# Kernel optimization log

Hardware: AMD Instinct MI355X
Metric: run time of the kernel (lower is better)

The kernel has to match this reference:

```python
import jax, jax.numpy as jnp
import numpy as np

N_NODES = 100000
N_EDGES = 1600000
HIDDEN = 128
N_CLASSES = 40
# torch.rand(1).item() in apply_randalign; fixed here for a deterministic reference
ALPHA = 0.62


def setup_inputs() -> dict:
    key = jax.random.key(0)
    ks = jax.random.split(key, 6)
    inputs = jax.random.normal(ks[0], (N_NODES, HIDDEN), jnp.float32)
    src = jax.random.randint(ks[1], (N_EDGES,), 0, N_NODES, jnp.int32)
    dst = jax.random.randint(ks[2], (N_EDGES,), 0, N_NODES, jnp.int32)
    s = 1.0 / np.sqrt(HIDDEN)
    W1 = jax.random.normal(ks[3], (HIDDEN, HIDDEN), jnp.float32) * s
    W2 = jax.random.normal(ks[4], (HIDDEN, HIDDEN), jnp.float32) * s
    W3 = jax.random.normal(ks[5], (HIDDEN, N_CLASSES), jnp.float32) * s
    return dict(inputs=inputs, src=src, dst=dst,
                W1=W1, b1=jnp.zeros((HIDDEN,), jnp.float32),
                W2=W2, b2=jnp.zeros((HIDDEN,), jnp.float32),
                W3=W3, b3=jnp.zeros((N_CLASSES,), jnp.float32))


def _graph_conv(x, W, b, src, dst):
    # DGL GraphConv, norm='both': D_dst^{-1/2} A D_src^{-1/2} X W + b
    n = x.shape[0]
    ones = jnp.ones(src.shape, x.dtype)
    deg_out = jnp.clip(jax.ops.segment_sum(ones, src, num_segments=n), 1.0)
    deg_in = jnp.clip(jax.ops.segment_sum(ones, dst, num_segments=n), 1.0)
    h = (x @ W) * (deg_out ** -0.5)[:, None]          # row scaling commutes with XW
    agg = jax.ops.segment_sum(h[src], dst, num_segments=n)
    return agg * (deg_in ** -0.5)[:, None] + b


def _randalign(h_prev, h_curr, alpha):
    norm_prev = jnp.linalg.norm(h_prev, axis=1, keepdims=True)
    norm_curr = jnp.linalg.norm(h_curr, axis=1, keepdims=True)
    scaled_prev = h_prev * (norm_curr / norm_prev)
    return alpha * h_curr + (1.0 - alpha) * scaled_prev


def reference(inputs, src, dst, W1, b1, W2, b2, W3, b3):
    # Faithful to source: layers[0] is never applied; loop runs over layers[1..-2].
    h = jax.nn.relu(_graph_conv(inputs, W1, b1, src, dst))      # i = 1
    h_next = jax.nn.relu(_graph_conv(h, W2, b2, src, dst))      # i = 2
    h = _randalign(h, h_next, ALPHA)
    logits = _graph_conv(h, W3, b3, src, dst)                   # final layer
    return logits
```

## Files before the change

kernel.cpp:

```cpp
#include <hip/hip_runtime.h>
#include <hip/hip_bf16.h>

#define HIDDEN 128
#define ALPHA_F 0.62f
#define CAP 64
#define BKT_BITS 9
#define BCAP 10240
#define CSTRIDE 136

typedef __attribute__((ext_vector_type(8))) short bf16x8;
typedef __attribute__((ext_vector_type(4))) float f32x4;

__device__ inline unsigned short f2bf(float f) {
  unsigned u = __float_as_uint(f);
  unsigned r = (u + 0x7fffu + ((u >> 16) & 1u)) >> 16;
  return (unsigned short)r;
}
__device__ inline float bf2f(unsigned short h) {
  return __uint_as_float((unsigned)h << 16);
}
__device__ inline float bflo(unsigned x) { return __uint_as_float(x << 16); }
__device__ inline float bfhi(unsigned x) { return __uint_as_float(x & 0xffff0000u); }
__device__ inline unsigned bfpack(float a, float b) {
  return (unsigned)f2bf(a) | ((unsigned)f2bf(b) << 16);
}

__device__ inline f32x4 mfma_bf16(bf16x8 a, bf16x8 b, f32x4 c) {
  return __builtin_amdgcn_mfma_f32_16x16x32_bf16(a, b, c, 0, 0, 0);
}

template <int CT>
__device__ void gemm_mfma_body(const float* __restrict__ A,
                               const unsigned short* __restrict__ WhT,
                               const unsigned short* __restrict__ WlT,
                               unsigned short* __restrict__ outp, int n, int NW, int gi,
                               unsigned* __restrict__ smem) {
  unsigned short* s16 = (unsigned short*)smem;
  const int t = threadIdx.x;
  const int wv = t >> 6, l = t & 63;
  const int lr = l & 15, lg = (l >> 4) & 3;
  const int rb = gi * 128;

  constexpr int WSLOTS = 4 * CT * 64;
  for (int s = t; s < WSLOTS; s += 256) {
    int sl = s & 63;
    int cc = s >> 6;
    int ct = cc % CT, c = cc / CT;
    int col = ct * 16 + (sl & 15);
    int k = c * 32 + ((sl >> 4) & 3) * 8;
    uint4 hv = *(const uint4*)&WhT[(size_t)col * HIDDEN + k];
    uint4 lv = *(const uint4*)&WlT[(size_t)col * HIDDEN + k];
    *(uint4*)&s16[(cc * 2 + 0) * 512 + sl * 8] = hv;
    *(uint4*)&s16[(cc * 2 + 1) * 512 + sl * 8] = lv;
  }

  f32x4 acc[2][CT];
#pragma unroll
  for (int rt = 0; rt < 2; rt++)
#pragma unroll
    for (int ct = 0; ct < CT; ct++)
#pragma unroll
      for (int e = 0; e < 4; e++) acc[rt][ct][e] = 0.f;

  __syncthreads();

  for (int c = 0; c < 4; c++) {
    bf16x8 ah[2], al[2];
#pragma unroll
    for (int rt = 0; rt < 2; rt++) {
      int rr = rb + wv * 32 + rt * 16 + lr;
      if (rr >= n) rr = n - 1;
      const float4* g = (const float4*)(A + (size_t)rr * HIDDEN + c * 32 + lg * 8);
      float4 v0 = g[0], v1 = g[1];
      float f[8] = {v0.x, v0.y, v0.z, v0.w, v1.x, v1.y, v1.z, v1.w};
#pragma unroll
      for (int q = 0; q < 8; q++) {
        unsigned short h = f2bf(f[q]);
        ah[rt][q] = (short)h;
        al[rt][q] = (short)f2bf(f[q] - bf2f(h));
      }
    }
#pragma unroll
    for (int ct = 0; ct < CT; ct++) {
      int cc = c * CT + ct;
      bf16x8 bh = *(const bf16x8*)&s16[(cc * 2 + 0) * 512 + l * 8];
      bf16x8 bl = *(const bf16x8*)&s16[(cc * 2 + 1) * 512 + l * 8];
#pragma unroll
      for (int rt = 0; rt < 2; rt++) {
        acc[rt][ct] = mfma_bf16(ah[rt], bh, acc[rt][ct]);
        acc[rt][ct] = mfma_bf16(al[rt], bh, acc[rt][ct]);
        acc[rt][ct] = mfma_bf16(ah[rt], bl, acc[rt][ct]);
      }
    }
  }

  __syncthreads();
  unsigned short* cr = s16 + wv * (32 * CSTRIDE);
#pragma unroll
  for (int rt = 0; rt < 2; rt++)
#pragma unroll
    for (int ct = 0; ct < CT; ct++)
#pragma unroll
      for (int r = 0; r < 4; r++)
        cr[(rt * 16 + lg * 4 + r) * CSTRIDE + ct * 16 + lr] = f2bf(acc[rt][ct][r]);
#pragma unroll
  for (int ps = 0; ps < 8; ps++) {
    int row_local = ps * 4 + lg;
    int orow = rb + wv * 32 + row_local;
    if (orow < n && lr * 8 < NW) {
      uint4 v = *(const uint4*)&cr[row_local * CSTRIDE + lr * 8];
      *(uint4*)&outp[(size_t)orow * NW + lr * 8] = v;
    }
  }
}

template <int CT>
__device__ void gemm_bf16A_body(const unsigned short* __restrict__ A,
                                const unsigned short* __restrict__ WhT,
                                const unsigned short* __restrict__ WlT,
                                unsigned short* __restrict__ outp, int n, int NW, int gi,
                                unsigned* __restrict__ smem) {
  unsigned short* s16 = (unsigned short*)smem;
  const int t = threadIdx.x;
  const int wv = t >> 6, l = t & 63;
  const int lr = l & 15, lg = (l >> 4) & 3;
  const int rb = gi * 128;

  constexpr int WSLOTS = 4 * CT * 64;
  for (int s = t; s < WSLOTS; s += 256) {
    int sl = s & 63;
    int cc = s >> 6;
    int ct = cc % CT, c = cc / CT;
    int col = ct * 16 + (sl & 15);
    int k = c * 32 + ((sl >> 4) & 3) * 8;
    uint4 hv = *(const uint4*)&WhT[(size_t)col * HIDDEN + k];
    uint4 lv = *(const uint4*)&WlT[(size_t)col * HIDDEN + k];
    *(uint4*)&s16[(cc * 2 + 0) * 512 + sl * 8] = hv;
    *(uint4*)&s16[(cc * 2 + 1) * 512 + sl * 8] = lv;
  }

  f32x4 acc[2][CT];
#pragma unroll
  for (int rt = 0; rt < 2; rt++)
#pragma unroll
    for (int ct = 0; ct < CT; ct++)
#pragma unroll
      for (int e = 0; e < 4; e++) acc[rt][ct][e] = 0.f;

  __syncthreads();

  for (int c = 0; c < 4; c++) {
    bf16x8 ah[2];
#pragma unroll
    for (int rt = 0; rt < 2; rt++) {
      int rr = rb + wv * 32 + rt * 16 + lr;
      if (rr >= n) rr = n - 1;
      ah[rt] = *(const bf16x8*)&A[(size_t)rr * HIDDEN + c * 32 + lg * 8];
    }
#pragma unroll
    for (int ct = 0; ct < CT; ct++) {
      int cc = c * CT + ct;
      bf16x8 bh = *(const bf16x8*)&s16[(cc * 2 + 0) * 512 + l * 8];
      bf16x8 bl = *(const bf16x8*)&s16[(cc * 2 + 1) * 512 + l * 8];
#pragma unroll
      for (int rt = 0; rt < 2; rt++) {
        acc[rt][ct] = mfma_bf16(ah[rt], bh, acc[rt][ct]);
        acc[rt][ct] = mfma_bf16(ah[rt], bl, acc[rt][ct]);
      }
    }
  }

  __syncthreads();
  unsigned short* cr = s16 + wv * (32 * CSTRIDE);
#pragma unroll
  for (int rt = 0; rt < 2; rt++)
#pragma unroll
    for (int ct = 0; ct < CT; ct++)
#pragma unroll
      for (int r = 0; r < 4; r++)
        cr[(rt * 16 + lg * 4 + r) * CSTRIDE + ct * 16 + lr] = f2bf(acc[rt][ct][r]);
#pragma unroll
  for (int ps = 0; ps < 8; ps++) {
    int row_local = ps * 4 + lg;
    int orow = rb + wv * 32 + row_local;
    if (orow < n && lr * 8 < NW) {
      uint4 v = *(const uint4*)&cr[row_local * CSTRIDE + lr * 8];
      *(uint4*)&outp[(size_t)orow * NW + lr * 8] = v;
    }
  }
}

__global__ __launch_bounds__(256) void partition_kernel(
    const int* __restrict__ src, const int* __restrict__ dst, int E, int nbkt,
    unsigned* __restrict__ gcur1, unsigned* __restrict__ gcur2,
    unsigned* __restrict__ stg1, unsigned short* __restrict__ stg2, int pa_blocks,
    const float* __restrict__ W1, const float* __restrict__ W2, const float* __restrict__ W3,
    unsigned short* __restrict__ W1h, unsigned short* __restrict__ W1l,
    unsigned short* __restrict__ W2h, unsigned short* __restrict__ W2l,
    unsigned short* __restrict__ W3h, unsigned short* __restrict__ W3l, int NC) {
  const int t = threadIdx.x;
  const int bid = blockIdx.x;
  if (bid >= pa_blocks) {
    int r = bid - pa_blocks;
    const float* W = (r == 0) ? W1 : (r == 1) ? W2 : W3;
    unsigned short* Wh = (r == 0) ? W1h : (r == 1) ? W2h : W3h;
    unsigned short* Wl = (r == 0) ? W1l : (r == 1) ? W2l : W3l;
    int ncol = (r == 2) ? 64 : 128;
    int nw   = (r == 2) ? NC : 128;
    for (int idx = t; idx < ncol * HIDDEN; idx += 256) {
      int c = idx >> 7, k = idx & 127;
      float v = (c < nw) ? W[(size_t)k * nw + c] : 0.f;
      unsigned short hi = f2bf(v);
      Wh[idx] = hi;
      Wl[idx] = f2bf(v - bf2f(hi));
    }
    return;
  }
  __shared__ unsigned h1[256], h2[256], b1[256], b2[256];
  h1[t] = 0; h2[t] = 0;
  __syncthreads();
  const int chunk = (E + pa_blocks - 1) / pa_blocks;
  const int e0 = bid * chunk, e1 = min(e0 + chunk, E);
  for (int e = e0 + t; e < e1; e += 256) {
    atomicAdd(&h1[(unsigned)dst[e] >> BKT_BITS], 1u);
    atomicAdd(&h2[(unsigned)src[e] >> BKT_BITS], 1u);
  }
  __syncthreads();
  if (t < nbkt) {
    b1[t] = atomicAdd(&gcur1[t], h1[t]);
    b2[t] = atomicAdd(&gcur2[t], h2[t]);
  }
  h1[t] = 0; h2[t] = 0;
  __syncthreads();
  for (int e = e0 + t; e < e1; e += 256) {
    int s = src[e], d = dst[e];
    unsigned bk1 = (unsigned)d >> BKT_BITS;
    unsigned p1 = b1[bk1] + atomicAdd(&h1[bk1], 1u);
    if (p1 < BCAP) stg1[(size_t)bk1 * BCAP + p1] = ((unsigned)s << BKT_BITS) | ((unsigned)d & 511u);
    unsigned bk2 = (unsigned)s >> BKT_BITS;
    unsigned p2 = b2[bk2] + atomicAdd(&h2[bk2], 1u);
    if (p2 < BCAP) stg2[(size_t)bk2 * BCAP + p2] = (unsigned short)(s & 511);
  }
}

__global__ __launch_bounds__(256) void csr_and_gemm1_kernel(
    const unsigned* __restrict__ gcur1, const unsigned* __restrict__ gcur2,
    const unsigned* __restrict__ stg1, const unsigned short* __restrict__ stg2,
    int* __restrict__ csr, int* __restrict__ deg_in, int* __restrict__ deg_out,
    int n, int nbkt,
    const float* __restrict__ X,
    const unsigned short* __restrict__ W1h, const unsigned short* __restrict__ W1l,
    unsigned short* __restrict__ T1) {
  __shared__ __align__(16) unsigned smem[16384];
  const int bid = blockIdx.x;
  if (bid >= 2 * nbkt) {
    gemm_mfma_body<8>(X, W1h, W1l, T1, n, HIDDEN, bid - 2 * nbkt, smem);
    return;
  }
  int* cnt = (int*)smem;
  const int t = threadIdx.x;
  cnt[t] = 0; cnt[t + 256] = 0;
  __syncthreads();
  if (bid < nbkt) {
    const int b = bid;
    const int m = min((int)gcur1[b], BCAP);
    const int node0 = b << BKT_BITS;
    for (int i = t; i < m; i += 256) {
      unsigned val = stg1[(size_t)b * BCAP + i];
      int dl = val & 511;
      int s = (int)(val >> BKT_BITS);
      int pos = atomicAdd(&cnt[dl], 1);
      if (pos < CAP) csr[((size_t)(node0 + dl) << 6) + pos] = s;
    }
    __syncthreads();
    for (int u = t; u < 512; u += 256) {
      int node = node0 + u;
      if (node < n) deg_in[node] = cnt[u];
    }
  } else {
    const int b = bid - nbkt;
    const int m = min((int)gcur2[b], BCAP);
    const int node0 = b << BKT_BITS;
    for (int i = t; i < m; i += 256) {
      atomicAdd(&cnt[stg2[(size_t)b * BCAP + i]], 1);
    }
    __syncthreads();
    for (int u = t; u < 512; u += 256) {
      int node = node0 + u;
      if (node < n) deg_out[node] = cnt[u];
    }
  }
}

__global__ __launch_bounds__(256) void gemm2_kernel(
    const unsigned short* __restrict__ A,
    const unsigned short* __restrict__ Wh, const unsigned short* __restrict__ Wl,
    unsigned short* __restrict__ T, int n) {
  __shared__ __align__(16) unsigned smem[16384];
  gemm_bf16A_body<8>(A, Wh, Wl, T, n, HIDDEN, blockIdx.x, smem);
}

__global__ __launch_bounds__(256) void gemm3_kernel(
    const unsigned short* __restrict__ A,
    const unsigned short* __restrict__ Wh, const unsigned short* __restrict__ Wl,
    unsigned short* __restrict__ T, int n) {
  __shared__ __align__(16) unsigned smem[9000];
  gemm_bf16A_body<4>(A, Wh, Wl, T, n, 64, blockIdx.x, smem);
}

template <bool RA>
__global__ __launch_bounds__(256) void gather_conv_kernel(
    const uint4* __restrict__ Tr, const int* __restrict__ csr,
    const int* __restrict__ deg_out, const int* __restrict__ deg_in,
    const float* __restrict__ bias, unsigned short* H, int n) {
  const int wv = threadIdx.x >> 6, l = threadIdx.x & 63;
  const int v = blockIdx.x * 4 + wv;
  if (v >= n) return;
  const int q = l >> 4, cg = l & 15;
  const int deg = deg_in[v];
  const int m = min(deg, CAP);
  int iu = (l < m) ? csr[((size_t)v << 6) + l] : 0;
  float wu = (l < m) ? rsqrtf((float)max(deg_out[iu], 1)) : 0.f;

  float a0 = 0.f, a1 = 0.f, a2 = 0.f, a3 = 0.f, a4 = 0.f, a5 = 0.f, a6 = 0.f, a7 = 0.f;
  float b0 = 0.f, b1 = 0.f, b2 = 0.f, b3 = 0.f, b4 = 0.f, b5 = 0.f, b6 = 0.f, b7 = 0.f;
  int j = 0;
  for (; j + 8 <= m; j += 8) {
    int eA = j + q, eB = j + 4 + q;
    int uA = __shfl(iu, eA), uB = __shfl(iu, eB);
    float wA = __shfl(wu, eA), wB = __shfl(wu, eB);
    uint4 xA = Tr[(size_t)uA * 16 + cg];
    uint4 xB = Tr[(size_t)uB * 16 + cg];
    a0 = fmaf(wA, bflo(xA.x), a0); a1 = fmaf(wA, bfhi(xA.x), a1);
    a2 = fmaf(wA, bflo(xA.y), a2); a3 = fmaf(wA, bfhi(xA.y), a3);
    a4 = fmaf(wA, bflo(xA.z), a4); a5 = fmaf(wA, bfhi(xA.z), a5);
    a6 = fmaf(wA, bflo(xA.w), a6); a7 = fmaf(wA, bfhi(xA.w), a7);
    b0 = fmaf(wB, bflo(xB.x), b0); b1 = fmaf(wB, bfhi(xB.x), b1);
    b2 = fmaf(wB, bflo(xB.y), b2); b3 = fmaf(wB, bfhi(xB.y), b3);
    b4 = fmaf(wB, bflo(xB.z), b4); b5 = fmaf(wB, bfhi(xB.z), b5);
    b6 = fmaf(wB, bflo(xB.w), b6); b7 = fmaf(wB, bfhi(xB.w), b7);
  }
  for (; j < m; j += 4) {
    int e = j + q;
    int u = __shfl(iu, e);
    float w = __shfl(wu, e);
    uint4 x = Tr[(size_t)u * 16 + cg];
    a0 = fmaf(w, bflo(x.x), a0); a1 = fmaf(w, bfhi(x.x), a1);
    a2 = fmaf(w, bflo(x.y), a2); a3 = fmaf(w, bfhi(x.y), a3);
    a4 = fmaf(w, bflo(x.z), a4); a5 = fmaf(w, bfhi(x.z), a5);
    a6 = fmaf(w, bflo(x.w), a6); a7 = fmaf(w, bfhi(x.w), a7);
  }
  a0 += b0; a1 += b1; a2 += b2; a3 += b3; a4 += b4; a5 += b5; a6 += b6; a7 += b7;
#pragma unroll
  for (int off = 16; off < 64; off <<= 1) {
    a0 += __shfl_xor(a0, off); a1 += __shfl_xor(a1, off);
    a2 += __shfl_xor(a2, off); a3 += __shfl_xor(a3, off);
    a4 += __shfl_xor(a4, off); a5 += __shfl_xor(a5, off);
    a6 += __shfl_xor(a6, off); a7 += __shfl_xor(a7, off);
  }

  float din = rsqrtf((float)max(deg, 1));
  float4 bA = ((const float4*)bias)[cg * 2];
  float4 bB = ((const float4*)bias)[cg * 2 + 1];
  float r0 = fmaxf(a0 * din + bA.x, 0.f);
  float r1 = fmaxf(a1 * din + bA.y, 0.f);
  float r2 = fmaxf(a2 * din + bA.z, 0.f);
  float r3 = fmaxf(a3 * din + bA.w, 0.f);
  float r4 = fmaxf(a4 * din + bB.x, 0.f);
  float r5 = fmaxf(a5 * din + bB.y, 0.f);
  float r6 = fmaxf(a6 * din + bB.z, 0.f);
  float r7 = fmaxf(a7 * din + bB.w, 0.f);

  if (RA) {
    uint4 hp = ((const uint4*)(H + (size_t)v * HIDDEN))[cg];
    float p0 = bflo(hp.x), p1 = bfhi(hp.x), p2 = bflo(hp.y), p3 = bfhi(hp.y);
    float p4 = bflo(hp.z), p5 = bfhi(hp.z), p6 = bflo(hp.w), p7 = bfhi(hp.w);
    float sc = r0*r0 + r1*r1 + r2*r2 + r3*r3 + r4*r4 + r5*r5 + r6*r6 + r7*r7;
    float sp = p0*p0 + p1*p1 + p2*p2 + p3*p3 + p4*p4 + p5*p5 + p6*p6 + p7*p7;
#pragma unroll
    for (int off = 1; off < 16; off <<= 1) {
      sc += __shfl_xor(sc, off);
      sp += __shfl_xor(sp, off);
    }
    float ratio = sqrtf(sc) / sqrtf(sp);
    const float am = 1.0f - ALPHA_F;
    r0 = ALPHA_F * r0 + am * p0 * ratio; r1 = ALPHA_F * r1 + am * p1 * ratio;
    r2 = ALPHA_F * r2 + am * p2 * ratio; r3 = ALPHA_F * r3 + am * p3 * ratio;
    r4 = ALPHA_F * r4 + am * p4 * ratio; r5 = ALPHA_F * r5 + am * p5 * ratio;
    r6 = ALPHA_F * r6 + am * p6 * ratio; r7 = ALPHA_F * r7 + am * p7 * ratio;
  }
  if (q == 0) {
    uint4 pk = make_uint4(bfpack(r0, r1), bfpack(r2, r3), bfpack(r4, r5), bfpack(r6, r7));
    ((uint4*)(H + (size_t)v * HIDDEN))[cg] = pk;
  }
}

__global__ __launch_bounds__(256) void gather_final_kernel(
    const uint4* __restrict__ Tr3, const int* __restrict__ csr,
    const int* __restrict__ deg_out, const int* __restrict__ deg_in,
    const float* __restrict__ bias, float* __restrict__ out, int n, int NC) {
  const int wv = threadIdx.x >> 6, l = threadIdx.x & 63;
  const int v = blockIdx.x * 4 + wv;
  if (v >= n) return;
  const int o = l >> 3, cg = l & 7;
  const int deg = deg_in[v];
  const int m = min(deg, CAP);
  int iu = (l < m) ? csr[((size_t)v << 6) + l] : 0;
  float wu = (l < m) ? rsqrtf((float)max(deg_out[iu], 1)) : 0.f;

  float a0 = 0.f, a1 = 0.f, a2 = 0.f, a3 = 0.f, a4 = 0.f, a5 = 0.f, a6 = 0.f, a7 = 0.f;
  float b0 = 0.f, b1 = 0.f, b2 = 0.f, b3 = 0.f, b4 = 0.f, b5 = 0.f, b6 = 0.f, b7 = 0.f;
  int j = 0;
  for (; j + 16 <= m; j += 16) {
    int eA = j + o, eB = j + 8 + o;
    int uA = __shfl(iu, eA), uB = __shfl(iu, eB);
    float wA = __shfl(wu, eA), wB = __shfl(wu, eB);
    uint4 xA = Tr3[(size_t)uA * 8 + cg];
    uint4 xB = Tr3[(size_t)uB * 8 + cg];
    a0 = fmaf(wA, bflo(xA.x), a0); a1 = fmaf(wA, bfhi(xA.x), a1);
    a2 = fmaf(wA, bflo(xA.y), a2); a3 = fmaf(wA, bfhi(xA.y), a3);
    a4 = fmaf(wA, bflo(xA.z), a4); a5 = fmaf(wA, bfhi(xA.z), a5);
    a6 = fmaf(wA, bflo(xA.w), a6); a7 = fmaf(wA, bfhi(xA.w), a7);
    b0 = fmaf(wB, bflo(xB.x), b0); b1 = fmaf(wB, bfhi(xB.x), b1);
    b2 = fmaf(wB, bflo(xB.y), b2); b3 = fmaf(wB, bfhi(xB.y), b3);
    b4 = fmaf(wB, bflo(xB.z), b4); b5 = fmaf(wB, bfhi(xB.z), b5);
    b6 = fmaf(wB, bflo(xB.w), b6); b7 = fmaf(wB, bfhi(xB.w), b7);
  }
  for (; j < m; j += 8) {
    int e = j + o;
    int u = __shfl(iu, e);
    float w = __shfl(wu, e);
    uint4 x = Tr3[(size_t)u * 8 + cg];
    a0 = fmaf(w, bflo(x.x), a0); a1 = fmaf(w, bfhi(x.x), a1);
    a2 = fmaf(w, bflo(x.y), a2); a3 = fmaf(w, bfhi(x.y), a3);
    a4 = fmaf(w, bflo(x.z), a4); a5 = fmaf(w, bfhi(x.z), a5);
    a6 = fmaf(w, bflo(x.w), a6); a7 = fmaf(w, bfhi(x.w), a7);
  }
  a0 += b0; a1 += b1; a2 += b2; a3 += b3; a4 += b4; a5 += b5; a6 += b6; a7 += b7;
#pragma unroll
  for (int off = 8; off < 64; off <<= 1) {
    a0 += __shfl_xor(a0, off); a1 += __shfl_xor(a1, off);
    a2 += __shfl_xor(a2, off); a3 += __shfl_xor(a3, off);
    a4 += __shfl_xor(a4, off); a5 += __shfl_xor(a5, off);
    a6 += __shfl_xor(a6, off); a7 += __shfl_xor(a7, off);
  }
  if (l < 5) {
    float din = rsqrtf((float)max(deg, 1));
    float4 bA = ((const float4*)bias)[l * 2];
    float4 bB = ((const float4*)bias)[l * 2 + 1];
    float4 oA = make_float4(a0 * din + bA.x, a1 * din + bA.y, a2 * din + bA.z, a3 * din + bA.w);
    float4 oB = make_float4(a4 * din + bB.x, a5 * din + bB.y, a6 * din + bB.z, a7 * din + bB.w);
    *(float4*)(out + (size_t)v * NC + 8 * l) = oA;
    *(float4*)(out + (size_t)v * NC + 8 * l + 4) = oB;
  }
}

extern "C" void kernel_launch(void* const* d_in, const int* in_sizes, int n_in,
                              void* d_out, int out_size, void* d_ws, size_t ws_size,
                              hipStream_t stream) {
  const float* X  = (const float*)d_in[0];
  const int* src  = (const int*)d_in[1];
  const int* dst  = (const int*)d_in[2];
  const float* W1 = (const float*)d_in[3];
  const float* b1 = (const float*)d_in[4];
  const float* W2 = (const float*)d_in[5];
  const float* b2 = (const float*)d_in[6];
  const float* W3 = (const float*)d_in[7];
  const float* b3 = (const float*)d_in[8];
  float* out = (float*)d_out;

  const int n = in_sizes[0] / HIDDEN;
  const int E = in_sizes[1];
  const int NC = in_sizes[8];
  const int nbkt = (n + 511) >> BKT_BITS;

  char* p = (char*)d_ws;
  auto alloc = [&](size_t bytes) {
    char* r = p;
    p += (bytes + 255) & ~(size_t)255;
    return r;
  };
  unsigned* gcur1 = (unsigned*)alloc(512 * 4);
  unsigned* gcur2 = gcur1 + 256;
  int* deg_out    = (int*)alloc((size_t)n * 4);
  int* deg_in     = (int*)alloc((size_t)n * 4);
  int* csr        = (int*)alloc((size_t)n * CAP * 4);
  unsigned short* stg2 = (unsigned short*)alloc((size_t)256 * BCAP * 2);
  unsigned* stg1  = (unsigned*)alloc((size_t)256 * BCAP * 4);
  unsigned short* BufT = (unsigned short*)alloc((size_t)n * HIDDEN * 2);
  unsigned short* BufH = (unsigned short*)alloc((size_t)n * HIDDEN * 2);
  unsigned short* W1h = (unsigned short*)alloc(128 * 128 * 2);
  unsigned short* W1l = (unsigned short*)alloc(128 * 128 * 2);
  unsigned short* W2h = (unsigned short*)alloc(128 * 128 * 2);
  unsigned short* W2l = (unsigned short*)alloc(128 * 128 * 2);
  unsigned short* W3h = (unsigned short*)alloc(64 * 128 * 2);
  unsigned short* W3l = (unsigned short*)alloc(64 * 128 * 2);

  hipMemsetAsync(gcur1, 0, 512 * 4, stream);

  const int PA = 256;
  partition_kernel<<<PA + 3, 256, 0, stream>>>(src, dst, E, nbkt, gcur1, gcur2, stg1, stg2, PA,
                                               W1, W2, W3, W1h, W1l, W2h, W2l, W3h, W3l, NC);

  int gb = (n + 127) / 128;
  csr_and_gemm1_kernel<<<2 * nbkt + gb, 256, 0, stream>>>(gcur1, gcur2, stg1, stg2,
                                                          csr, deg_in, deg_out, n, nbkt,
                                                          X, W1h, W1l, BufT);
  int hb = (n + 3) / 4;
  gather_conv_kernel<false><<<hb, 256, 0, stream>>>(
      (const uint4*)BufT, csr, deg_out, deg_in, b1, BufH, n);
  gemm2_kernel<<<gb, 256, 0, stream>>>(BufH, W2h, W2l, BufT, n);
  gather_conv_kernel<true><<<hb, 256, 0, stream>>>(
      (const uint4*)BufT, csr, deg_out, deg_in, b2, BufH, n);
  gemm3_kernel<<<gb, 256, 0, stream>>>(BufH, W3h, W3l, BufT, n);
  gather_final_kernel<<<hb, 256, 0, stream>>>(
      (const uint4*)BufT, csr, deg_out, deg_in, b3, out, n, NC);
}
```

Baseline: 277.5 us.

## Fold source-degree scaling into GEMM epilogues and rework gathers to per-edge wave loads

Adds a kernel that precomputes per-node deg_out^-1/2 once. The gemm2 and gemm3 epilogues now apply that scale to rows before storing, so the layer-2 and layer-3 gathers become plain sums. The gather kernels are restructured so the whole wave reads one neighbor row per step, with the index broadcast via readlane, instead of splitting lanes across edges and reducing with shuffles. This removes per-edge rsqrt work and the cross-lane reductions, but each wave now issues narrower 4-byte or 2-byte loads per edge with less memory-level parallelism. It also adds one extra launch.

```diff
diff --git a/kernel.cpp b/kernel.cpp
--- a/kernel.cpp
+++ b/kernel.cpp
@@ -118,6 +118,7 @@
 __device__ void gemm_bf16A_body(const unsigned short* __restrict__ A,
                                 const unsigned short* __restrict__ WhT,
                                 const unsigned short* __restrict__ WlT,
+                                const float* __restrict__ dsc,
                                 unsigned short* __restrict__ outp, int n, int NW, int gi,
                                 unsigned* __restrict__ smem) {
   unsigned short* s16 = (unsigned short*)smem;
@@ -173,12 +174,16 @@
   __syncthreads();
   unsigned short* cr = s16 + wv * (32 * CSTRIDE);
 #pragma unroll
-  for (int rt = 0; rt < 2; rt++)
-#pragma unroll
-    for (int ct = 0; ct < CT; ct++)
-#pragma unroll
-      for (int r = 0; r < 4; r++)
-        cr[(rt * 16 + lg * 4 + r) * CSTRIDE + ct * 16 + lr] = f2bf(acc[rt][ct][r]);
+  for (int rt = 0; rt < 2; rt++) {
+#pragma unroll
+    for (int r = 0; r < 4; r++) {
+      int orow = rb + wv * 32 + rt * 16 + lg * 4 + r;
+      float sc = dsc[min(orow, n - 1)];
+#pragma unroll
+      for (int ct = 0; ct < CT; ct++)
+        cr[(rt * 16 + lg * 4 + r) * CSTRIDE + ct * 16 + lr] = f2bf(acc[rt][ct][r] * sc);
+    }
+  }
 #pragma unroll
   for (int ps = 0; ps < 8; ps++) {
     int row_local = ps * 4 + lg;
@@ -292,166 +297,126 @@
   }
 }
 
+__global__ __launch_bounds__(256) void dscale_kernel(const int* __restrict__ deg_out,
+                                                     float* __restrict__ dscale, int n) {
+  int i = blockIdx.x * 256 + threadIdx.x;
+  if (i < n) dscale[i] = rsqrtf((float)max(deg_out[i], 1));
+}
+
 __global__ __launch_bounds__(256) void gemm2_kernel(
     const unsigned short* __restrict__ A,
     const unsigned short* __restrict__ Wh, const unsigned short* __restrict__ Wl,
-    unsigned short* __restrict__ T, int n) {
+    const float* __restrict__ dsc, unsigned short* __restrict__ T, int n) {
   __shared__ __align__(16) unsigned smem[16384];
-  gemm_bf16A_body<8>(A, Wh, Wl, T, n, HIDDEN, blockIdx.x, smem);
+  gemm_bf16A_body<8>(A, Wh, Wl, dsc, T, n, HIDDEN, blockIdx.x, smem);
 }
 
 __global__ __launch_bounds__(256) void gemm3_kernel(
     const unsigned short* __restrict__ A,
     const unsigned short* __restrict__ Wh, const unsigned short* __restrict__ Wl,
-    unsigned short* __restrict__ T, int n) {
+    const float* __restrict__ dsc, unsigned short* __restrict__ T, int n) {
   __shared__ __align__(16) unsigned smem[9000];
-  gemm_bf16A_body<4>(A, Wh, Wl, T, n, 64, blockIdx.x, smem);
-}
-
-template <bool RA>
+  gemm_bf16A_body<4>(A, Wh, Wl, dsc, T, n, 64, blockIdx.x, smem);
+}
+
+template <bool APPLYW, bool RA>
 __global__ __launch_bounds__(256) void gather_conv_kernel(
-    const uint4* __restrict__ Tr, const int* __restrict__ csr,
-    const int* __restrict__ deg_out, const int* __restrict__ deg_in,
+    const unsigned* __restrict__ Tu, const int* __restrict__ csr,
+    const float* __restrict__ dscale, const int* __restrict__ deg_in,
     const float* __restrict__ bias, unsigned short* H, int n) {
-  const int wv = threadIdx.x >> 6, l = threadIdx.x & 63;
-  const int v = blockIdx.x * 4 + wv;
+  const int l = threadIdx.x & 63;
+  const int v = __builtin_amdgcn_readfirstlane(blockIdx.x * 4 + (threadIdx.x >> 6));
   if (v >= n) return;
-  const int q = l >> 4, cg = l & 15;
   const int deg = deg_in[v];
   const int m = min(deg, CAP);
   int iu = (l < m) ? csr[((size_t)v << 6) + l] : 0;
-  float wu = (l < m) ? rsqrtf((float)max(deg_out[iu], 1)) : 0.f;
-
-  float a0 = 0.f, a1 = 0.f, a2 = 0.f, a3 = 0.f, a4 = 0.f, a5 = 0.f, a6 = 0.f, a7 = 0.f;
-  float b0 = 0.f, b1 = 0.f, b2 = 0.f, b3 = 0.f, b4 = 0.f, b5 = 0.f, b6 = 0.f, b7 = 0.f;
-  int j = 0;
-  for (; j + 8 <= m; j += 8) {
-    int eA = j + q, eB = j + 4 + q;
-    int uA = __shfl(iu, eA), uB = __shfl(iu, eB);
-    float wA = __shfl(wu, eA), wB = __shfl(wu, eB);
-    uint4 xA = Tr[(size_t)uA * 16 + cg];
-    uint4 xB = Tr[(size_t)uB * 16 + cg];
-    a0 = fmaf(wA, bflo(xA.x), a0); a1 = fmaf(wA, bfhi(xA.x), a1);
-    a2 = fmaf(wA, bflo(xA.y), a2); a3 = fmaf(wA, bfhi(xA.y), a3);
-    a4 = fmaf(wA, bflo(xA.z), a4); a5 = fmaf(wA, bfhi(xA.z), a5);
-    a6 = fmaf(wA, bflo(xA.w), a6); a7 = fmaf(wA, bfhi(xA.w), a7);
-    b0 = fmaf(wB, bflo(xB.x), b0); b1 = fmaf(wB, bfhi(xB.x), b1);
-    b2 = fmaf(wB, bflo(xB.y), b2); b3 = fmaf(wB, bfhi(xB.y), b3);
-    b4 = fmaf(wB, bflo(xB.z), b4); b5 = fmaf(wB, bfhi(xB.z), b5);
-    b6 = fmaf(wB, bflo(xB.w), b6); b7 = fmaf(wB, bfhi(xB.w), b7);
-  }
-  for (; j < m; j += 4) {
-    int e = j + q;
-    int u = __shfl(iu, e);
-    float w = __shfl(wu, e);
-    uint4 x = Tr[(size_t)u * 16 + cg];
-    a0 = fmaf(w, bflo(x.x), a0); a1 = fmaf(w, bfhi(x.x), a1);
-    a2 = fmaf(w, bflo(x.y), a2); a3 = fmaf(w, bfhi(x.y), a3);
-    a4 = fmaf(w, bflo(x.z), a4); a5 = fmaf(w, bfhi(x.z), a5);
-    a6 = fmaf(w, bflo(x.w), a6); a7 = fmaf(w, bfhi(x.w), a7);
-  }
-  a0 += b0; a1 += b1; a2 += b2; a3 += b3; a4 += b4; a5 += b5; a6 += b6; a7 += b7;
-#pragma unroll
-  for (int off = 16; off < 64; off <<= 1) {
-    a0 += __shfl_xor(a0, off); a1 += __shfl_xor(a1, off);
-    a2 += __shfl_xor(a2, off); a3 += __shfl_xor(a3, off);
-    a4 += __shfl_xor(a4, off); a5 += __shfl_xor(a5, off);
-    a6 += __shfl_xor(a6, off); a7 += __shfl_xor(a7, off);
-  }
+
+  float acc0 = 0.f, acc1 = 0.f, acc2 = 0.f, acc3 = 0.f;
+  int jb = 0;
+  for (; jb + 8 <= m; jb += 8) {
+#pragma unroll
+    for (int jj = 0; jj < 8; jj += 2) {
+      int uA = __builtin_amdgcn_readlane(iu, jb + jj);
+      int uB = __builtin_amdgcn_readlane(iu, jb + jj + 1);
+      unsigned xA = Tu[(size_t)uA * 64 + l];
+      unsigned xB = Tu[(size_t)uB * 64 + l];
+      if (APPLYW) {
+        float wA = dscale[uA], wB = dscale[uB];
+        acc0 = fmaf(wA, bflo(xA), acc0); acc1 = fmaf(wA, bfhi(xA), acc1);
+        acc2 = fmaf(wB, bflo(xB), acc2); acc3 = fmaf(wB, bfhi(xB), acc3);
+      } else {
+        acc0 += bflo(xA); acc1 += bfhi(xA);
+        acc2 += bflo(xB); acc3 += bfhi(xB);
+      }
+    }
+  }
+  for (; jb < m; jb++) {
+    int u = __builtin_amdgcn_readlane(iu, jb);
+    unsigned x = Tu[(size_t)u * 64 + l];
+    if (APPLYW) {
+      float w = dscale[u];
+      acc0 = fmaf(w, bflo(x), acc0); acc1 = fmaf(w, bfhi(x), acc1);
+    } else {
+      acc0 += bflo(x); acc1 += bfhi(x);
+    }
+  }
+  acc0 += acc2; acc1 += acc3;
 
   float din = rsqrtf((float)max(deg, 1));
-  float4 bA = ((const float4*)bias)[cg * 2];
-  float4 bB = ((const float4*)bias)[cg * 2 + 1];
-  float r0 = fmaxf(a0 * din + bA.x, 0.f);
-  float r1 = fmaxf(a1 * din + bA.y, 0.f);
-  float r2 = fmaxf(a2 * din + bA.z, 0.f);
-  float r3 = fmaxf(a3 * din + bA.w, 0.f);
-  float r4 = fmaxf(a4 * din + bB.x, 0.f);
-  float r5 = fmaxf(a5 * din + bB.y, 0.f);
-  float r6 = fmaxf(a6 * din + bB.z, 0.f);
-  float r7 = fmaxf(a7 * din + bB.w, 0.f);
+  float2 b2 = ((const float2*)bias)[l];
+  float r0 = fmaxf(acc0 * din + b2.x, 0.f);
+  float r1 = fmaxf(acc1 * din + b2.y, 0.f);
 
   if (RA) {
-    uint4 hp = ((const uint4*)(H + (size_t)v * HIDDEN))[cg];
-    float p0 = bflo(hp.x), p1 = bfhi(hp.x), p2 = bflo(hp.y), p3 = bfhi(hp.y);
-    float p4 = bflo(hp.z), p5 = bfhi(hp.z), p6 = bflo(hp.w), p7 = bfhi(hp.w);
-    float sc = r0*r0 + r1*r1 + r2*r2 + r3*r3 + r4*r4 + r5*r5 + r6*r6 + r7*r7;
-    float sp = p0*p0 + p1*p1 + p2*p2 + p3*p3 + p4*p4 + p5*p5 + p6*p6 + p7*p7;
-#pragma unroll
-    for (int off = 1; off < 16; off <<= 1) {
+    unsigned hp = ((const unsigned*)H)[(size_t)v * 64 + l];
+    float p0 = bflo(hp), p1 = bfhi(hp);
+    float sc = r0 * r0 + r1 * r1;
+    float sp = p0 * p0 + p1 * p1;
+#pragma unroll
+    for (int off = 1; off < 64; off <<= 1) {
       sc += __shfl_xor(sc, off);
       sp += __shfl_xor(sp, off);
     }
     float ratio = sqrtf(sc) / sqrtf(sp);
     const float am = 1.0f - ALPHA_F;
-    r0 = ALPHA_F * r0 + am * p0 * ratio; r1 = ALPHA_F * r1 + am * p1 * ratio;
-    r2 = ALPHA_F * r2 + am * p2 * ratio; r3 = ALPHA_F * r3 + am * p3 * ratio;
-    r4 = ALPHA_F * r4 + am * p4 * ratio; r5 = ALPHA_F * r5 + am * p5 * ratio;
-    r6 = ALPHA_F * r6 + am * p6 * ratio; r7 = ALPHA_F * r7 + am * p7 * ratio;
-  }
-  if (q == 0) {
-    uint4 pk = make_uint4(bfpack(r0, r1), bfpack(r2, r3), bfpack(r4, r5), bfpack(r6, r7));
-    ((uint4*)(H + (size_t)v * HIDDEN))[cg] = pk;
-  }
+    r0 = ALPHA_F * r0 + am * p0 * ratio;
+    r1 = ALPHA_F * r1 + am * p1 * ratio;
+  }
+  ((unsigned*)H)[(size_t)v * 64 + l] = bfpack(r0, r1);
 }
 
 __global__ __launch_bounds__(256) void gather_final_kernel(
-    const uint4* __restrict__ Tr3, const int* __restrict__ csr,
-    const int* __restrict__ deg_out, const int* __restrict__ deg_in,
-    const float* __restrict__ bias, float* __restrict__ out, int n, int NC) {
-  const int wv = threadIdx.x >> 6, l = threadIdx.x & 63;
-  const int v = blockIdx.x * 4 + wv;
+    const unsigned short* __restrict__ T3, const int* __restrict__ csr,
+    const int* __restrict__ deg_in, const float* __restrict__ bias,
+    float* __restrict__ out, int n, int NC) {
+  const int l = threadIdx.x & 63;
+  const int v = __builtin_amdgcn_readfirstlane(blockIdx.x * 4 + (threadIdx.x >> 6));
   if (v >= n) return;
-  const int o = l >> 3, cg = l & 7;
   const int deg = deg_in[v];
   const int m = min(deg, CAP);
   int iu = (l < m) ? csr[((size_t)v << 6) + l] : 0;
-  float wu = (l < m) ? rsqrtf((float)max(deg_out[iu], 1)) : 0.f;
-
-  float a0 = 0.f, a1 = 0.f, a2 = 0.f, a3 = 0.f, a4 = 0.f, a5 = 0.f, a6 = 0.f, a7 = 0.f;
-  float b0 = 0.f, b1 = 0.f, b2 = 0.f, b3 = 0.f, b4 = 0.f, b5 = 0.f, b6 = 0.f, b7 = 0.f;
-  int j = 0;
-  for (; j + 16 <= m; j += 16) {
-    int eA = j + o, eB = j + 8 + o;
-    int uA = __shfl(iu, eA), uB = __shfl(iu, eB);
-    float wA = __shfl(wu, eA), wB = __shfl(wu, eB);
-    uint4 xA = Tr3[(size_t)uA * 8 + cg];
-    uint4 xB = Tr3[(size_t)uB * 8 + cg];
-    a0 = fmaf(wA, bflo(xA.x), a0); a1 = fmaf(wA, bfhi(xA.x), a1);
-    a2 = fmaf(wA, bflo(xA.y), a2); a3 = fmaf(wA, bfhi(xA.y), a3);
-    a4 = fmaf(wA, bflo(xA.z), a4); a5 = fmaf(wA, bfhi(xA.z), a5);
-    a6 = fmaf(wA, bflo(xA.w), a6); a7 = fmaf(wA, bfhi(xA.w), a7);
-    b0 = fmaf(wB, bflo(xB.x), b0); b1 = fmaf(wB, bfhi(xB.x), b1);
-    b2 = fmaf(wB, bflo(xB.y), b2); b3 = fmaf(wB, bfhi(xB.y), b3);
-    b4 = fmaf(wB, bflo(xB.z), b4); b5 = fmaf(wB, bfhi(xB.z), b5);
-    b6 = fmaf(wB, bflo(xB.w), b6); b7 = fmaf(wB, bfhi(xB.w), b7);
-  }
-  for (; j < m; j += 8) {
-    int e = j + o;
-    int u = __shfl(iu, e);
-    float w = __shfl(wu, e);
-    uint4 x = Tr3[(size_t)u * 8 + cg];
-    a0 = fmaf(w, bflo(x.x), a0); a1 = fmaf(w, bfhi(x.x), a1);
-    a2 = fmaf(w, bflo(x.y), a2); a3 = fmaf(w, bfhi(x.y), a3);
-    a4 = fmaf(w, bflo(x.z), a4); a5 = fmaf(w, bfhi(x.z), a5);
-    a6 = fmaf(w, bflo(x.w), a6); a7 = fmaf(w, bfhi(x.w), a7);
-  }
-  a0 += b0; a1 += b1; a2 += b2; a3 += b3; a4 += b4; a5 += b5; a6 += b6; a7 += b7;
-#pragma unroll
-  for (int off = 8; off < 64; off <<= 1) {
-    a0 += __shfl_xor(a0, off); a1 += __shfl_xor(a1, off);
-    a2 += __shfl_xor(a2, off); a3 += __shfl_xor(a3, off);
-    a4 += __shfl_xor(a4, off); a5 += __shfl_xor(a5, off);
-    a6 += __shfl_xor(a6, off); a7 += __shfl_xor(a7, off);
-  }
-  if (l < 5) {
+
+  float acc0 = 0.f, acc1 = 0.f;
+  int jb = 0;
+  for (; jb + 8 <= m; jb += 8) {
+#pragma unroll
+    for (int jj = 0; jj < 8; jj += 2) {
+      int uA = __builtin_amdgcn_readlane(iu, jb + jj);
+      int uB = __builtin_amdgcn_readlane(iu, jb + jj + 1);
+      unsigned short xA = T3[(size_t)uA * 64 + l];
+      unsigned short xB = T3[(size_t)uB * 64 + l];
+      acc0 += bf2f(xA);
+      acc1 += bf2f(xB);
+    }
+  }
+  for (; jb < m; jb++) {
+    int u = __builtin_amdgcn_readlane(iu, jb);
+    acc0 += bf2f(T3[(size_t)u * 64 + l]);
+  }
+  acc0 += acc1;
+  if (l < 40) {
     float din = rsqrtf((float)max(deg, 1));
-    float4 bA = ((const float4*)bias)[l * 2];
-    float4 bB = ((const float4*)bias)[l * 2 + 1];
-    float4 oA = make_float4(a0 * din + bA.x, a1 * din + bA.y, a2 * din + bA.z, a3 * din + bA.w);
-    float4 oB = make_float4(a4 * din + bB.x, a5 * din + bB.y, a6 * din + bB.z, a7 * din + bB.w);
-    *(float4*)(out + (size_t)v * NC + 8 * l) = oA;
-    *(float4*)(out + (size_t)v * NC + 8 * l + 4) = oB;
+    out[(size_t)v * NC + l] = acc0 * din + bias[l];
   }
 }
 
@@ -484,6 +449,7 @@
   unsigned* gcur2 = gcur1 + 256;
   int* deg_out    = (int*)alloc((size_t)n * 4);
   int* deg_in     = (int*)alloc((size_t)n * 4);
+  float* dscale   = (float*)alloc((size_t)n * 4);
   int* csr        = (int*)alloc((size_t)n * CAP * 4);
   unsigned short* stg2 = (unsigned short*)alloc((size_t)256 * BCAP * 2);
   unsigned* stg1  = (unsigned*)alloc((size_t)256 * BCAP * 4);
@@ -506,13 +472,16 @@
   csr_and_gemm1_kernel<<<2 * nbkt + gb, 256, 0, stream>>>(gcur1, gcur2, stg1, stg2,
                                                           csr, deg_in, deg_out, n, nbkt,
                                                           X, W1h, W1l, BufT);
+  int nb = (n + 255) / 256;
+  dscale_kernel<<<nb, 256, 0, stream>>>(deg_out, dscale, n);
+
   int hb = (n + 3) / 4;
-  gather_conv_kernel<false><<<hb, 256, 0, stream>>>(
-      (const uint4*)BufT, csr, deg_out, deg_in, b1, BufH, n);
-  gemm2_kernel<<<gb, 256, 0, stream>>>(BufH, W2h, W2l, BufT, n);
-  gather_conv_kernel<true><<<hb, 256, 0, stream>>>(
-      (const uint4*)BufT, csr, deg_out, deg_in, b2, BufH, n);
-  gemm3_kernel<<<gb, 256, 0, stream>>>(BufH, W3h, W3l, BufT, n);
+  gather_conv_kernel<true, false><<<hb, 256, 0, stream>>>(
+      (const unsigned*)BufT, csr, dscale, deg_in, b1, BufH, n);
+  gemm2_kernel<<<gb, 256, 0, stream>>>(BufH, W2h, W2l, dscale, BufT, n);
+  gather_conv_kernel<false, true><<<hb, 256, 0, stream>>>(
+      (const unsigned*)BufT, csr, dscale, deg_in, b2, BufH, n);
+  gemm3_kernel<<<gb, 256, 0, stream>>>(BufH, W3h, W3l, dscale, BufT, n);
   gather_final_kernel<<<hb, 256, 0, stream>>>(
-      (const uint4*)BufT, csr, deg_out, deg_in, b3, out, n, NC);
-}
+      (const unsigned short*)BufT, csr, deg_in, b3, out, n, NC);
+}
```

Result: slower. 285.5 us (+2.9%).
